# Performance work log

Hardware: AMD Instinct MI355X
Metric: run time of the kernel (lower is better)

The kernel has to match this reference:

```python
import math
import jax, jax.numpy as jnp
import numpy as np

S = 30.0          # cfg.MODEL.HEADS.SCALE
M = 0.5           # cfg.MODEL.HEADS.MARGIN
MOM = 0.5         # EMA momentum (hardcoded in module)
COS_M = math.cos(M)
SIN_M = math.sin(M)
THRESHOLD = math.cos(math.pi - M)
MM = math.sin(math.pi - M) * M
EPS = 1e-12       # F.normalize eps


def setup_inputs() -> dict:
    key = jax.random.key(0)
    k1, k2, k3 = jax.random.split(key, 3)
    B, D, C = 512, 256, 100000
    features = jax.random.normal(k1, (B, D), jnp.float32)
    targets = jax.random.randint(k2, (B,), 0, C, dtype=jnp.int32).astype(jnp.int64)
    weight = jax.random.normal(k3, (C, D), jnp.float32)
    weight = weight / jnp.maximum(jnp.linalg.norm(weight, axis=1, keepdims=True), EPS)
    t = jnp.zeros((1,), jnp.float32)
    return {"features": features, "targets": targets, "weight": weight, "t": t}


def reference(features, targets, weight, t):
    B = features.shape[0]
    C = weight.shape[0]
    rows = jnp.arange(B)

    # F.normalize(features, dim=1)
    f = features / jnp.maximum(jnp.linalg.norm(features, axis=1, keepdims=True), EPS)

    # cos_theta = f @ W.T   [B, C]
    cos_theta = jnp.einsum('bd,cd->bc', f, weight)

    # ArcFace margin on the target logit
    target_logit = cos_theta[rows, targets][:, None]              # [B, 1]
    sin_theta = jnp.sqrt(jnp.maximum(1.0 - target_logit ** 2, 0.0))
    cos_theta_m = target_logit * COS_M - sin_theta * SIN_M        # cos(theta + m)
    mask = cos_theta > cos_theta_m                                 # hard examples
    final_target_logit = jnp.where(target_logit > THRESHOLD,
                                   cos_theta_m, target_logit - MM)

    # EMA of mean target logit (buffer t), used immediately after update
    t_new = jnp.mean(target_logit) * 0.01 + 0.99 * t              # [1]

    # hard-example reweighting: cos[mask] = hard * (t + hard)
    cos_theta = jnp.where(mask, cos_theta * (t_new[0] + cos_theta), cos_theta)
    # scatter final target logit into the target column
    cos_theta = cos_theta.at[rows, targets].set(final_target_logit[:, 0])

    pred_class_logits = cos_theta * S

    # memory-bank EMA update: per-unique-target mean, EMA, renormalize (no_grad)
    fd = jax.lax.stop_gradient(f)
    counts = jax.ops.segment_sum(jnp.ones((B,), fd.dtype), targets, num_segments=C)
    sums = jax.ops.segment_sum(fd, targets, num_segments=C)        # [C, D]
    mean_w = sums / jnp.maximum(counts, 1.0)[:, None]
    upd = MOM * weight + (1.0 - MOM) * mean_w
    upd = upd / jnp.maximum(jnp.linalg.norm(upd, axis=1, keepdims=True), EPS)
    new_weight = jnp.where((counts > 0)[:, None], upd, weight)

    return pred_class_logits, new_weight, t_new
```

## Files before the change

kernel.cpp:

```cpp
#include <hip/hip_runtime.h>
#include <math.h>

#define B_SZ 512
#define D_SZ 256
#define C_SZ 100000
#define S_SCALE 30.0f
#define COS_Mc 0.8775825618903728f
#define SIN_Mc 0.479425538604203f
#define THRESHOLDc (-0.8775825618903728f)
#define MMc 0.2397127693021015f
#define EPSc 1e-12f

#define OUT_W_OFF ((size_t)B_SZ * C_SZ)
#define OUT_T_OFF (OUT_W_OFF + (size_t)C_SZ * D_SZ)

#define WS_F 0
#define WS_TL (B_SZ * D_SZ)
#define WS_CTM (WS_TL + B_SZ)
#define WS_FLT (WS_CTM + B_SZ)
#define WS_TNEW (WS_FLT + B_SZ)

typedef __attribute__((ext_vector_type(8))) short bf16x8;
typedef __attribute__((ext_vector_type(4))) short s16x4;
typedef __attribute__((ext_vector_type(4))) float f32x4;

__device__ __forceinline__ float wave_reduce_sum(float v) {
#pragma unroll
    for (int off = 32; off > 0; off >>= 1) v += __shfl_down(v, off, 64);
    return v;
}

__device__ __forceinline__ short f2bf(float x) {
    union { float f; unsigned u; } v; v.f = x;
    unsigned r = v.u + 0x7fff + ((v.u >> 16) & 1);
    return (short)(r >> 16);
}
__device__ __forceinline__ float bf2f(short h) {
    union { float f; unsigned u; } v;
    v.u = ((unsigned)(unsigned short)h) << 16;
    return v.f;
}

__global__ __launch_bounds__(256) void prep_kernel(
    const float* __restrict__ features, const int* __restrict__ targets,
    const float* __restrict__ weight, float* __restrict__ f,
    float* __restrict__ tl, float* __restrict__ ctm, float* __restrict__ flt) {
    int b = blockIdx.x;
    int d = threadIdx.x;
    float x = features[b * D_SZ + d];
    float v = wave_reduce_sum(x * x);
    __shared__ float red[4];
    int wave = d >> 6, lane = d & 63;
    if (lane == 0) red[wave] = v;
    __syncthreads();
    float s = red[0] + red[1] + red[2] + red[3];
    float scale = 1.0f / fmaxf(sqrtf(s), EPSc);
    float fv = x * scale;
    f[b * D_SZ + d] = fv;

    int tgt = targets[b];
    float wv = weight[(size_t)tgt * D_SZ + d];
    float p = wave_reduce_sum(fv * wv);
    __syncthreads();
    if (lane == 0) red[wave] = p;
    __syncthreads();
    if (d == 0) {
        float t_l = red[0] + red[1] + red[2] + red[3];
        tl[b] = t_l;
        float sin_t = sqrtf(fmaxf(1.0f - t_l * t_l, 0.0f));
        float c_m = t_l * COS_Mc - sin_t * SIN_Mc;
        ctm[b] = c_m;
        flt[b] = (t_l > THRESHOLDc) ? c_m : (t_l - MMc);
    }
}

__global__ __launch_bounds__(512) void tnew_kernel(
    const float* __restrict__ tl, const float* __restrict__ t_in,
    float* __restrict__ tnew_ws, float* __restrict__ out_t) {
    int i = threadIdx.x;
    float v = wave_reduce_sum(tl[i]);
    __shared__ float red[8];
    int wave = i >> 6, lane = i & 63;
    if (lane == 0) red[wave] = v;
    __syncthreads();
    if (i == 0) {
        float s = 0.f;
#pragma unroll
        for (int w = 0; w < 8; w++) s += red[w];
        float tn = (s / (float)B_SZ) * 0.01f + 0.99f * t_in[0];
        tnew_ws[0] = tn;
        out_t[0] = tn;
    }
}

#define BMt 128
#define BNt 128
#define LDK 40

__global__ __launch_bounds__(256) void gemm_kernel(
    const float* __restrict__ f, const float* __restrict__ weight,
    const int* __restrict__ targets, const float* __restrict__ ctm,
    const float* __restrict__ flt, const float* __restrict__ tnew,
    float* __restrict__ out) {
    __shared__ short As_hi[BMt][LDK];
    __shared__ short As_lo[BMt][LDK];
    __shared__ short Bs_hi[BNt][LDK];
    __shared__ short Bs_lo[BNt][LDK];

    const int t = threadIdx.x;
    const int row0 = blockIdx.y * BMt;
    const int col0 = blockIdx.x * BNt;
    const int w = t >> 6, lane = t & 63;
    const int wr = w >> 1, wc = w & 1;
    const int fr = lane & 15;
    const int kg = (lane >> 4) * 8;

    f32x4 acc[4][4] = {};

    for (int kt = 0; kt < D_SZ; kt += 32) {
#pragma unroll
        for (int i = 0; i < 4; i++) {
            int flat = i * 256 + t;
            int m = flat >> 3;
            int kq = flat & 7;
            float4 va = *(const float4*)&f[(row0 + m) * D_SZ + kt + kq * 4];
            s16x4 h, l;
            h.x = f2bf(va.x); l.x = f2bf(va.x - bf2f(h.x));
            h.y = f2bf(va.y); l.y = f2bf(va.y - bf2f(h.y));
            h.z = f2bf(va.z); l.z = f2bf(va.z - bf2f(h.z));
            h.w = f2bf(va.w); l.w = f2bf(va.w - bf2f(h.w));
            *(s16x4*)&As_hi[m][kq * 4] = h;
            *(s16x4*)&As_lo[m][kq * 4] = l;
            int c = col0 + m;
            float4 vb = make_float4(0.f, 0.f, 0.f, 0.f);
            if (c < C_SZ) vb = *(const float4*)&weight[(size_t)c * D_SZ + kt + kq * 4];
            h.x = f2bf(vb.x); l.x = f2bf(vb.x - bf2f(h.x));
            h.y = f2bf(vb.y); l.y = f2bf(vb.y - bf2f(h.y));
            h.z = f2bf(vb.z); l.z = f2bf(vb.z - bf2f(h.z));
            h.w = f2bf(vb.w); l.w = f2bf(vb.w - bf2f(h.w));
            *(s16x4*)&Bs_hi[m][kq * 4] = h;
            *(s16x4*)&Bs_lo[m][kq * 4] = l;
        }
        __syncthreads();

        bf16x8 ah[4], al[4], bh[4], bl[4];
#pragma unroll
        for (int mi = 0; mi < 4; mi++) {
            int m = wr * 64 + mi * 16 + fr;
            ah[mi] = *(const bf16x8*)&As_hi[m][kg];
            al[mi] = *(const bf16x8*)&As_lo[m][kg];
        }
#pragma unroll
        for (int ni = 0; ni < 4; ni++) {
            int c = wc * 64 + ni * 16 + fr;
            bh[ni] = *(const bf16x8*)&Bs_hi[c][kg];
            bl[ni] = *(const bf16x8*)&Bs_lo[c][kg];
        }
#pragma unroll
        for (int mi = 0; mi < 4; mi++)
#pragma unroll
            for (int ni = 0; ni < 4; ni++) {
                acc[mi][ni] = __builtin_amdgcn_mfma_f32_16x16x32_bf16(
                    ah[mi], bh[ni], acc[mi][ni], 0, 0, 0);
                acc[mi][ni] = __builtin_amdgcn_mfma_f32_16x16x32_bf16(
                    ah[mi], bl[ni], acc[mi][ni], 0, 0, 0);
                acc[mi][ni] = __builtin_amdgcn_mfma_f32_16x16x32_bf16(
                    al[mi], bh[ni], acc[mi][ni], 0, 0, 0);
            }
        __syncthreads();
    }

    float tn = tnew[0];
#pragma unroll
    for (int mi = 0; mi < 4; mi++) {
#pragma unroll
        for (int j = 0; j < 4; j++) {
            int r = row0 + wr * 64 + mi * 16 + (lane >> 4) * 4 + j;
            int tg = targets[r];
            float cm = ctm[r], fl = flt[r];
            size_t base = (size_t)r * C_SZ;
#pragma unroll
            for (int ni = 0; ni < 4; ni++) {
                int c = col0 + wc * 64 + ni * 16 + fr;
                if (c < C_SZ) {
                    float v = acc[mi][ni][j];
                    if (c == tg) v = fl;
                    else if (v > cm) v = v * (tn + v);
                    out[base + c] = v * S_SCALE;
                }
            }
        }
    }
}

__global__ __launch_bounds__(256) void copyw_kernel(
    const float4* __restrict__ src, float4* __restrict__ dst, int n4) {
    int i = blockIdx.x * blockDim.x + threadIdx.x;
    if (i < n4) dst[i] = src[i];
}

__global__ __launch_bounds__(256) void updw_kernel(
    const int* __restrict__ targets, const float* __restrict__ f,
    const float* __restrict__ weight, float* __restrict__ outw) {
    int b = blockIdx.x;
    int c = targets[b];
    for (int i = 0; i < b; i++)
        if (targets[i] == c) return;
    int d = threadIdx.x;
    float sum = 0.f;
    int cnt = 0;
    for (int i = b; i < B_SZ; i++) {
        if (targets[i] == c) { sum += f[i * D_SZ + d]; cnt++; }
    }
    float mean = sum / (float)cnt;
    float upd = 0.5f * weight[(size_t)c * D_SZ + d] + 0.5f * mean;
    float v = wave_reduce_sum(upd * upd);
    __shared__ float red[4];
    int wave = d >> 6, lane = d & 63;
    if (lane == 0) red[wave] = v;
    __syncthreads();
    float s = red[0] + red[1] + red[2] + red[3];
    float nrm = fmaxf(sqrtf(s), EPSc);
    outw[(size_t)c * D_SZ + d] = upd / nrm;
}

extern "C" void kernel_launch(void* const* d_in, const int* in_sizes, int n_in,
                              void* d_out, int out_size, void* d_ws, size_t ws_size,
                              hipStream_t stream) {
    const float* features = (const float*)d_in[0];
    const int* targets = (const int*)d_in[1];
    const float* weight = (const float*)d_in[2];
    const float* t_in = (const float*)d_in[3];
    float* out = (float*)d_out;
    float* ws = (float*)d_ws;

    float* f = ws + WS_F;
    float* tl = ws + WS_TL;
    float* ctm = ws + WS_CTM;
    float* flt = ws + WS_FLT;
    float* tnew = ws + WS_TNEW;

    prep_kernel<<<B_SZ, 256, 0, stream>>>(features, targets, weight, f, tl, ctm, flt);
    tnew_kernel<<<1, 512, 0, stream>>>(tl, t_in, tnew, out + OUT_T_OFF);

    int n4 = (C_SZ * D_SZ) / 4;
    copyw_kernel<<<(n4 + 255) / 256, 256, 0, stream>>>(
        (const float4*)weight, (float4*)(out + OUT_W_OFF), n4);

    dim3 ggrid((C_SZ + BNt - 1) / BNt, B_SZ / BMt);
    gemm_kernel<<<ggrid, 256, 0, stream>>>(f, weight, targets, ctm, flt, tnew, out);

    updw_kernel<<<B_SZ, 256, 0, stream>>>(targets, f, weight, out + OUT_W_OFF);
}
```

Baseline: 626.1 us.

## Pre-split operands into bf16 hi/lo buffers and load MFMA fragments directly from global

Adds a pack kernel that converts the weight matrix once into separate bf16 hi and lo arrays, staged in the new-weight output region before that region is overwritten by the copy. The prep kernel does the same for the normalized features. The GEMM then reads MFMA fragments straight from global memory with no LDS staging or barriers, using 64-column tiles where each wave covers 64 rows. This removes the per-tile float-to-bf16 split work and the LDS round trip, at the cost of an extra pass over the weight matrix and possibly less reuse, since each block now covers only 64 columns. The update kernel also caches targets in shared memory and uses a parallel duplicate check.

```diff
diff --git a/kernel.cpp b/kernel.cpp
--- a/kernel.cpp
+++ b/kernel.cpp
@@ -14,14 +14,15 @@
 #define OUT_W_OFF ((size_t)B_SZ * C_SZ)
 #define OUT_T_OFF (OUT_W_OFF + (size_t)C_SZ * D_SZ)
 
-#define WS_F 0
-#define WS_TL (B_SZ * D_SZ)
-#define WS_CTM (WS_TL + B_SZ)
-#define WS_FLT (WS_CTM + B_SZ)
-#define WS_TNEW (WS_FLT + B_SZ)
+#define WSB_F 0
+#define WSB_FHI 524288
+#define WSB_FLO 786432
+#define WSB_TL 1048576
+#define WSB_CTM 1050624
+#define WSB_FLT 1052672
+#define WSB_TNEW 1054720
 
 typedef __attribute__((ext_vector_type(8))) short bf16x8;
-typedef __attribute__((ext_vector_type(4))) short s16x4;
 typedef __attribute__((ext_vector_type(4))) float f32x4;
 
 __device__ __forceinline__ float wave_reduce_sum(float v) {
@@ -30,20 +31,21 @@
     return v;
 }
 
-__device__ __forceinline__ short f2bf(float x) {
+__device__ __forceinline__ unsigned short f2bf(float x) {
     union { float f; unsigned u; } v; v.f = x;
     unsigned r = v.u + 0x7fff + ((v.u >> 16) & 1);
-    return (short)(r >> 16);
-}
-__device__ __forceinline__ float bf2f(short h) {
+    return (unsigned short)(r >> 16);
+}
+__device__ __forceinline__ float bf2f(unsigned short h) {
     union { float f; unsigned u; } v;
-    v.u = ((unsigned)(unsigned short)h) << 16;
+    v.u = ((unsigned)h) << 16;
     return v.f;
 }
 
 __global__ __launch_bounds__(256) void prep_kernel(
     const float* __restrict__ features, const int* __restrict__ targets,
     const float* __restrict__ weight, float* __restrict__ f,
+    unsigned short* __restrict__ fhi, unsigned short* __restrict__ flo,
     float* __restrict__ tl, float* __restrict__ ctm, float* __restrict__ flt) {
     int b = blockIdx.x;
     int d = threadIdx.x;
@@ -57,6 +59,9 @@
     float scale = 1.0f / fmaxf(sqrtf(s), EPSc);
     float fv = x * scale;
     f[b * D_SZ + d] = fv;
+    unsigned short h = f2bf(fv);
+    fhi[b * D_SZ + d] = h;
+    flo[b * D_SZ + d] = f2bf(fv - bf2f(h));
 
     int tgt = targets[b];
     float wv = weight[(size_t)tgt * D_SZ + d];
@@ -93,68 +98,71 @@
     }
 }
 
-#define BMt 128
-#define BNt 128
-#define LDK 40
+__global__ __launch_bounds__(256) void wpack_kernel(
+    const float* __restrict__ w, unsigned short* __restrict__ whi,
+    unsigned short* __restrict__ wlo) {
+    size_t i = ((size_t)blockIdx.x * 256 + threadIdx.x) * 8;
+    float4 a = *(const float4*)&w[i];
+    float4 b = *(const float4*)&w[i + 4];
+    union { unsigned short us[8]; bf16x8 v; } h, l;
+    float xs[8] = {a.x, a.y, a.z, a.w, b.x, b.y, b.z, b.w};
+#pragma unroll
+    for (int j = 0; j < 8; j++) {
+        unsigned short hh = f2bf(xs[j]);
+        h.us[j] = hh;
+        l.us[j] = f2bf(xs[j] - bf2f(hh));
+    }
+    *(bf16x8*)&whi[i] = h.v;
+    *(bf16x8*)&wlo[i] = l.v;
+}
 
 __global__ __launch_bounds__(256) void gemm_kernel(
-    const float* __restrict__ f, const float* __restrict__ weight,
+    const unsigned short* __restrict__ fhi, const unsigned short* __restrict__ flo,
+    const unsigned short* __restrict__ whi, const unsigned short* __restrict__ wlo,
     const int* __restrict__ targets, const float* __restrict__ ctm,
     const float* __restrict__ flt, const float* __restrict__ tnew,
     float* __restrict__ out) {
-    __shared__ short As_hi[BMt][LDK];
-    __shared__ short As_lo[BMt][LDK];
-    __shared__ short Bs_hi[BNt][LDK];
-    __shared__ short Bs_lo[BNt][LDK];
-
     const int t = threadIdx.x;
-    const int row0 = blockIdx.y * BMt;
-    const int col0 = blockIdx.x * BNt;
     const int w = t >> 6, lane = t & 63;
-    const int wr = w >> 1, wc = w & 1;
     const int fr = lane & 15;
     const int kg = (lane >> 4) * 8;
+    const int col0 = blockIdx.x * 64;
+    const int row0 = blockIdx.y * 256 + w * 64;
+
+    bool nval[4];
+#pragma unroll
+    for (int ni = 0; ni < 4; ni++) nval[ni] = (col0 + ni * 16) < C_SZ;
+
+    const unsigned short* arow[4];
+    const unsigned short* brow[4];
+#pragma unroll
+    for (int mi = 0; mi < 4; mi++)
+        arow[mi] = fhi + (size_t)(row0 + mi * 16 + fr) * D_SZ + kg;
+#pragma unroll
+    for (int ni = 0; ni < 4; ni++)
+        brow[ni] = whi + (size_t)(col0 + ni * 16 + fr) * D_SZ + kg;
+    const size_t dlo_f = (size_t)(flo - fhi);
+    const size_t dlo_w = (size_t)(wlo - whi);
 
     f32x4 acc[4][4] = {};
 
+#pragma unroll 2
     for (int kt = 0; kt < D_SZ; kt += 32) {
-#pragma unroll
-        for (int i = 0; i < 4; i++) {
-            int flat = i * 256 + t;
-            int m = flat >> 3;
-            int kq = flat & 7;
-            float4 va = *(const float4*)&f[(row0 + m) * D_SZ + kt + kq * 4];
-            s16x4 h, l;
-            h.x = f2bf(va.x); l.x = f2bf(va.x - bf2f(h.x));
-            h.y = f2bf(va.y); l.y = f2bf(va.y - bf2f(h.y));
-            h.z = f2bf(va.z); l.z = f2bf(va.z - bf2f(h.z));
-            h.w = f2bf(va.w); l.w = f2bf(va.w - bf2f(h.w));
-            *(s16x4*)&As_hi[m][kq * 4] = h;
-            *(s16x4*)&As_lo[m][kq * 4] = l;
-            int c = col0 + m;
-            float4 vb = make_float4(0.f, 0.f, 0.f, 0.f);
-            if (c < C_SZ) vb = *(const float4*)&weight[(size_t)c * D_SZ + kt + kq * 4];
-            h.x = f2bf(vb.x); l.x = f2bf(vb.x - bf2f(h.x));
-            h.y = f2bf(vb.y); l.y = f2bf(vb.y - bf2f(h.y));
-            h.z = f2bf(vb.z); l.z = f2bf(vb.z - bf2f(h.z));
-            h.w = f2bf(vb.w); l.w = f2bf(vb.w - bf2f(h.w));
-            *(s16x4*)&Bs_hi[m][kq * 4] = h;
-            *(s16x4*)&Bs_lo[m][kq * 4] = l;
+        bf16x8 ah[4], al[4], bh[4], bl[4];
+#pragma unroll
+        for (int mi = 0; mi < 4; mi++) {
+            ah[mi] = *(const bf16x8*)(arow[mi] + kt);
+            al[mi] = *(const bf16x8*)(arow[mi] + kt + dlo_f);
         }
-        __syncthreads();
-
-        bf16x8 ah[4], al[4], bh[4], bl[4];
-#pragma unroll
-        for (int mi = 0; mi < 4; mi++) {
-            int m = wr * 64 + mi * 16 + fr;
-            ah[mi] = *(const bf16x8*)&As_hi[m][kg];
-            al[mi] = *(const bf16x8*)&As_lo[m][kg];
-        }
 #pragma unroll
         for (int ni = 0; ni < 4; ni++) {
-            int c = wc * 64 + ni * 16 + fr;
-            bh[ni] = *(const bf16x8*)&Bs_hi[c][kg];
-            bl[ni] = *(const bf16x8*)&Bs_lo[c][kg];
+            if (nval[ni]) {
+                bh[ni] = *(const bf16x8*)(brow[ni] + kt);
+                bl[ni] = *(const bf16x8*)(brow[ni] + kt + dlo_w);
+            } else {
+                bh[ni] = (bf16x8)0;
+                bl[ni] = (bf16x8)0;
+            }
         }
 #pragma unroll
         for (int mi = 0; mi < 4; mi++)
@@ -167,7 +175,6 @@
                 acc[mi][ni] = __builtin_amdgcn_mfma_f32_16x16x32_bf16(
                     al[mi], bh[ni], acc[mi][ni], 0, 0, 0);
             }
-        __syncthreads();
     }
 
     float tn = tnew[0];
@@ -175,14 +182,14 @@
     for (int mi = 0; mi < 4; mi++) {
 #pragma unroll
         for (int j = 0; j < 4; j++) {
-            int r = row0 + wr * 64 + mi * 16 + (lane >> 4) * 4 + j;
+            int r = row0 + mi * 16 + (lane >> 4) * 4 + j;
             int tg = targets[r];
             float cm = ctm[r], fl = flt[r];
             size_t base = (size_t)r * C_SZ;
 #pragma unroll
             for (int ni = 0; ni < 4; ni++) {
-                int c = col0 + wc * 64 + ni * 16 + fr;
-                if (c < C_SZ) {
+                if (nval[ni]) {
+                    int c = col0 + ni * 16 + fr;
                     float v = acc[mi][ni][j];
                     if (c == tg) v = fl;
                     else if (v > cm) v = v * (tn + v);
@@ -202,26 +209,34 @@
 __global__ __launch_bounds__(256) void updw_kernel(
     const int* __restrict__ targets, const float* __restrict__ f,
     const float* __restrict__ weight, float* __restrict__ outw) {
+    __shared__ int tg[B_SZ];
+    __shared__ int dup;
+    int t = threadIdx.x;
+    if (t == 0) dup = 0;
+    tg[t] = targets[t];
+    tg[t + 256] = targets[t + 256];
+    __syncthreads();
     int b = blockIdx.x;
-    int c = targets[b];
-    for (int i = 0; i < b; i++)
-        if (targets[i] == c) return;
-    int d = threadIdx.x;
+    int c = tg[b];
+    if ((t < b && tg[t] == c) || (t + 256 < b && tg[t + 256] == c)) dup = 1;
+    __syncthreads();
+    if (dup) return;
+
     float sum = 0.f;
     int cnt = 0;
     for (int i = b; i < B_SZ; i++) {
-        if (targets[i] == c) { sum += f[i * D_SZ + d]; cnt++; }
+        if (tg[i] == c) { sum += f[i * D_SZ + t]; cnt++; }
     }
     float mean = sum / (float)cnt;
-    float upd = 0.5f * weight[(size_t)c * D_SZ + d] + 0.5f * mean;
+    float upd = 0.5f * weight[(size_t)c * D_SZ + t] + 0.5f * mean;
     float v = wave_reduce_sum(upd * upd);
     __shared__ float red[4];
-    int wave = d >> 6, lane = d & 63;
+    int wave = t >> 6, lane = t & 63;
     if (lane == 0) red[wave] = v;
     __syncthreads();
     float s = red[0] + red[1] + red[2] + red[3];
     float nrm = fmaxf(sqrtf(s), EPSc);
-    outw[(size_t)c * D_SZ + d] = upd / nrm;
+    outw[(size_t)c * D_SZ + t] = upd / nrm;
 }
 
 extern "C" void kernel_launch(void* const* d_in, const int* in_sizes, int n_in,
@@ -232,23 +247,32 @@
     const float* weight = (const float*)d_in[2];
     const float* t_in = (const float*)d_in[3];
     float* out = (float*)d_out;
-    float* ws = (float*)d_ws;
-
-    float* f = ws + WS_F;
-    float* tl = ws + WS_TL;
-    float* ctm = ws + WS_CTM;
-    float* flt = ws + WS_FLT;
-    float* tnew = ws + WS_TNEW;
-
-    prep_kernel<<<B_SZ, 256, 0, stream>>>(features, targets, weight, f, tl, ctm, flt);
+    char* wsb = (char*)d_ws;
+
+    float* f = (float*)(wsb + WSB_F);
+    unsigned short* fhi = (unsigned short*)(wsb + WSB_FHI);
+    unsigned short* flo = (unsigned short*)(wsb + WSB_FLO);
+    float* tl = (float*)(wsb + WSB_TL);
+    float* ctm = (float*)(wsb + WSB_CTM);
+    float* flt = (float*)(wsb + WSB_FLT);
+    float* tnew = (float*)(wsb + WSB_TNEW);
+
+    unsigned short* whi = (unsigned short*)(out + OUT_W_OFF);
+    unsigned short* wlo = whi + (size_t)C_SZ * D_SZ;
+
+    prep_kernel<<<B_SZ, 256, 0, stream>>>(features, targets, weight, f, fhi, flo,
+                                          tl, ctm, flt);
     tnew_kernel<<<1, 512, 0, stream>>>(tl, t_in, tnew, out + OUT_T_OFF);
+
+    wpack_kernel<<<12500, 256, 0, stream>>>(weight, whi, wlo);
+
+    dim3 ggrid((C_SZ + 63) / 64, 2);
+    gemm_kernel<<<ggrid, 256, 0, stream>>>(fhi, flo, whi, wlo, targets, ctm, flt,
+                                           tnew, out);
 
     int n4 = (C_SZ * D_SZ) / 4;
     copyw_kernel<<<(n4 + 255) / 256, 256, 0, stream>>>(
         (const float4*)weight, (float4*)(out + OUT_W_OFF), n4);
 
-    dim3 ggrid((C_SZ + BNt - 1) / BNt, B_SZ / BMt);
-    gemm_kernel<<<ggrid, 256, 0, stream>>>(f, weight, targets, ctm, flt, tnew, out);
-
     updw_kernel<<<B_SZ, 256, 0, stream>>>(targets, f, weight, out + OUT_W_OFF);
 }
```

New measurement: 738.9 us. +18.0%, slower.
